# Kernel optimization log

Hardware: AMD Instinct MI355X
Metric: run time of the kernel (lower is better)

Reference implementation:

```python
import jax, jax.numpy as jnp
import numpy as np

STRIDE = 25
TOPK = 3
EPS = 1e-9


def setup_inputs() -> dict:
    key = jax.random.key(0)
    k1, k2, k3, k4 = jax.random.split(key, 4)
    B, N, T, P = 128, 200, 360, 400
    x = jax.random.normal(k1, (B, N, T), dtype=jnp.float32)
    # per-sample time-series lengths; min 100 so size_after_pool >= 1
    length = jax.random.randint(k2, (B,), 100, T + 1)
    # xavier_uniform with gain=1.414 as in nn.init.xavier_uniform_(.., gain=1.414)
    limit = float(np.sqrt(6.0 / (P + N)) * 1.414)
    patterns = jax.random.uniform(k3, (P, N), minval=-limit, maxval=limit, dtype=jnp.float32)
    # simple linear classifier standing in for Baselines.mlp(num_of_node)
    W_cls = jax.random.normal(k4, (N * N, 2), dtype=jnp.float32) * 0.01
    b_cls = jnp.zeros((2,), dtype=jnp.float32)
    return {"x": x, "length": length, "patterns": patterns, "W_cls": W_cls, "b_cls": b_cls}


def _forward(x, length, patterns, W_cls, b_cls):
    B, N, T = x.shape
    P = patterns.shape[0]
    # size_after_pool = floor(length / stride)  [B]
    sap = (length // STRIDE).astype(jnp.int32)
    # MRI_length_regularize (random_start=False): the scatter-mask keeps
    # t < size_after_pool*stride per sample; padded tail is exactly zero and
    # contributes 0 through maxpool+sum, so static full-T masking is equivalent.
    valid = (jnp.arange(T)[None, :] < (sap * STRIDE)[:, None]).astype(x.dtype)  # [B,T]
    frames = (x * valid[:, None, :]).transpose(0, 2, 1)  # [B,T,N]
    nf = frames / jnp.sqrt((frames ** 2).sum(-1, keepdims=True) + EPS)
    npat = patterns / jnp.sqrt((patterns ** 2).sum(-1, keepdims=True) + EPS)
    # top_select: keep top-K |entries| per pattern row
    _, topi = jax.lax.top_k(jnp.abs(npat), TOPK)  # [P,K]
    pmask = jnp.zeros((P, N), x.dtype).at[jnp.arange(P)[:, None], topi].set(1.0)
    toppattern = pmask * npat
    # scores + strided max-pool over time
    scores = jnp.einsum('btn,pn->bpt', nf, npat)  # [B,P,T]
    nwin = T // STRIDE
    pos = scores[:, :, : nwin * STRIDE].reshape(B, P, nwin, STRIDE).max(-1)  # [B,P,nwin]
    finalscore = (pos / sap[:, None, None].astype(x.dtype)).sum(-1)  # [B,P]
    # realpattern = toppattern.detach(); graphs = R^T diag(finalscore) R / (maskgraph+eps)
    realpattern = jax.lax.stop_gradient(toppattern)
    maskgraph = pmask.T @ pmask  # [N,N]
    graphs = jnp.einsum('pn,bp,pm->bnm', realpattern, finalscore, realpattern) / (maskgraph + EPS)
    out = graphs.reshape(B, -1) @ W_cls + b_cls  # [B,2]
    # Critical_ROI(normalized_patterns, toppattern)
    norm = (((1.0 - jnp.linalg.norm(toppattern, axis=-1) / jnp.linalg.norm(npat, axis=-1)) ** 2).sum() / 800.0)
    rec = jnp.zeros((1,), x.dtype)
    return out, norm, rec


def reference(x, length, patterns, W_cls, b_cls):
    return _forward(x, length, patterns, W_cls, b_cls)
```

## Files before the change

### kernel.cpp

```cpp
#include <hip/hip_runtime.h>

#define N_NODE 200
#define T_LEN 360
#define T_POOL 350
#define P_PAT 400
#define P_PAD 512
#define NWIN 14
#define STRIDE_ 25
#define KPAD 224

#define O_AH    0
#define O_AL    229376
#define O_MG    458752
#define O_POS   618752
#define O_TOPN  4288768
#define O_TOPV  4293568
#define O_NORMT 4298368

typedef unsigned short u16;
typedef __attribute__((ext_vector_type(8))) short bf16x8;
typedef __attribute__((ext_vector_type(4))) float f32x4;

__device__ __forceinline__ unsigned fkey(float f) {
    unsigned u = __float_as_uint(f);
    return (u & 0x80000000u) ? ~u : (u | 0x80000000u);
}
__device__ __forceinline__ u16 f2bf(float f) {
    unsigned u = __float_as_uint(f);
    unsigned r = u + 0x7FFFu + ((u >> 16) & 1u);
    return (u16)(r >> 16);
}
__device__ __forceinline__ float bf2f(u16 h) { return __uint_as_float(((unsigned)h) << 16); }

__global__ void k_pat(const float* __restrict__ pat, u16* __restrict__ Ah, u16* __restrict__ Al,
                      int* __restrict__ mg, int* __restrict__ topn_w,
                      float* __restrict__ topv_w, float* __restrict__ normt,
                      unsigned* __restrict__ pos)
{
    int p = blockIdx.x;
    int lane = threadIdx.x;
    bool pv = p < P_PAT;

    {
        int base = blockIdx.x * 64 + lane;
        #pragma unroll
        for (int i = 0; i < 28; ++i) pos[base + i * 32768] = 0u;
    }

    float sv[4], av[4];
    int nn[4];
    float ss = 0.f;
    #pragma unroll
    for (int j = 0; j < 4; ++j) {
        int n = lane + 64 * j;
        nn[j] = n;
        if (pv && n < N_NODE) { float v = pat[p * N_NODE + n]; sv[j] = v; av[j] = fabsf(v); ss += v * v; }
        else { sv[j] = 0.f; av[j] = -1.f; }
    }
    #pragma unroll
    for (int off = 32; off >= 1; off >>= 1) ss += __shfl_xor(ss, off);
    float rn = 1.0f / sqrtf(ss + 1e-9f);

    int pb = p >> 6, ii = (p >> 4) & 3, plm = p & 15;
    #pragma unroll
    for (int j = 0; j < 4; ++j) {
        int n = nn[j];
        if (n < KPAD) {
            float v = (pv && n < N_NODE) ? sv[j] * rn : 0.f;
            u16 h = f2bf(v);
            u16 l = f2bf(v - bf2f(h));
            int s = n >> 5, c = n & 31, quad = c >> 3, e = c & 7;
            size_t idx = ((size_t)((s * 8 + pb) * 4 + ii) * 64 + quad * 16 + plm) * 8 + e;
            Ah[idx] = h; Al[idx] = l;
        }
    }
    if (!pv) return;

    int topn[3]; float topv[3];
    for (int r = 0; r < 3; ++r) {
        float bv = -2.f; int bi = 1 << 30;
        #pragma unroll
        for (int j = 0; j < 4; ++j)
            if (av[j] > bv || (av[j] == bv && nn[j] < bi)) { bv = av[j]; bi = nn[j]; }
        #pragma unroll
        for (int off = 32; off >= 1; off >>= 1) {
            float ov = __shfl_xor(bv, off); int oi = __shfl_xor(bi, off);
            if (ov > bv || (ov == bv && oi < bi)) { bv = ov; bi = oi; }
        }
        int jj = bi >> 6, src = bi & 63;
        float rawj = (jj == 0) ? sv[0] : (jj == 1) ? sv[1] : (jj == 2) ? sv[2] : sv[3];
        float raw = __shfl(rawj, src);
        topn[r] = bi; topv[r] = raw * rn;
        #pragma unroll
        for (int j = 0; j < 4; ++j) if (nn[j] == bi) av[j] = -1.f;
    }
    float fullnorm = sqrtf(ss) * rn;
    float topnorm = sqrtf(topv[0]*topv[0] + topv[1]*topv[1] + topv[2]*topv[2]);
    if (lane == 0) {
        float d = 1.0f - topnorm / fullnorm;
        normt[p] = d * d * (1.0f / 800.0f);
    }
    if (lane < 3) { topn_w[p * 3 + lane] = topn[lane]; topv_w[p * 3 + lane] = topv[lane]; }
    if (lane < 9) {
        int i = lane / 3, j = lane % 3;
        atomicAdd(&mg[topn[i] * N_NODE + topn[j]], 1);
    }
}

#define RP 2064
#define XLOFF 8256
#define DBS 16512
#define SQOFF 16896
#define IVOFF 18944
__global__ __launch_bounds__(256, 3) void k_gemm(const float* __restrict__ x,
    const u16* __restrict__ AhF, const u16* __restrict__ AlF,
    const int* __restrict__ length, unsigned* __restrict__ pos)
{
    __shared__ __align__(16) char smem[33024];
    int tid = threadIdx.x;
    int b = blockIdx.z, p0 = blockIdx.y * 128, t0 = blockIdx.x * 128;
    int lane = tid & 63, wid = tid >> 6;
    int quad = lane >> 4, lm = lane & 15;
    int wp = wid >> 1, wt = wid & 1;
    const float* xb = x + (size_t)b * (N_NODE * T_LEN);

    f32x4 acc[4][4];
    #pragma unroll
    for (int i = 0; i < 4; ++i)
        #pragma unroll
        for (int j = 0; j < 4; ++j) acc[i][j] = (f32x4){0.f, 0.f, 0.f, 0.f};
    float ssq0 = 0.f, ssq1 = 0.f;

    int tg = t0 + 2 * lane;
    bool tok = tg < T_LEN;
    int xfb = quad * RP + (lm & 1) * 1024 + (lm >> 1) * 16 + wt * 512;
    int pbq = blockIdx.y * 2 + wp;

    float2 xv[8];
    auto loadX = [&](int s) {
        int kb = s * 32 + wid * 8;
        #pragma unroll
        for (int e = 0; e < 8; ++e) {
            int k = kb + e;
            xv[e] = (tok && k < N_NODE) ? *(const float2*)(xb + k * T_LEN + tg)
                                        : make_float2(0.f, 0.f);
        }
    };
    auto cw = [&](int buf) {
        union { u16 us[8]; uint4 v; } H0, H1, L0, L1;
        #pragma unroll
        for (int e = 0; e < 8; ++e) {
            float f0 = xv[e].x, f1 = xv[e].y;
            ssq0 = fmaf(f0, f0, ssq0); ssq1 = fmaf(f1, f1, ssq1);
            u16 h = f2bf(f0); H0.us[e] = h; L0.us[e] = f2bf(f0 - bf2f(h));
            h = f2bf(f1);     H1.us[e] = h; L1.us[e] = f2bf(f1 - bf2f(h));
        }
        char* bp = smem + buf * DBS + wid * RP + lane * 16;
        *(uint4*)(bp)               = H0.v;
        *(uint4*)(bp + 1024)        = H1.v;
        *(uint4*)(bp + XLOFF)        = L0.v;
        *(uint4*)(bp + XLOFF + 1024) = L1.v;
    };

    loadX(0); cw(0);
    bf16x8 ah[4], al[4], xh[4], xl[4];
    for (int s = 0; s < 7; ++s) {
        const u16* Ab  = AhF + ((size_t)((s * 8 + pbq) * 4)) * 512 + lane * 8;
        const u16* Ab2 = AlF + ((size_t)((s * 8 + pbq) * 4)) * 512 + lane * 8;
        #pragma unroll
        for (int i = 0; i < 4; ++i) {
            ah[i] = *(const bf16x8*)(Ab  + i * 512);
            al[i] = *(const bf16x8*)(Ab2 + i * 512);
        }
        if (s < 6) loadX(s + 1);
        __syncthreads();
        const char* rb = smem + (s & 1) * DBS + xfb;
        #pragma unroll
        for (int j = 0; j < 4; ++j) {
            xh[j] = *(const bf16x8*)(rb + j * 128);
            xl[j] = *(const bf16x8*)(rb + XLOFF + j * 128);
        }
        #pragma unroll
        for (int i = 0; i < 4; ++i)
            #pragma unroll
            for (int j = 0; j < 4; ++j)
                acc[i][j] = __builtin_amdgcn_mfma_f32_16x16x32_bf16(ah[i], xh[j], acc[i][j], 0, 0, 0);
        #pragma unroll
        for (int i = 0; i < 4; ++i)
            #pragma unroll
            for (int j = 0; j < 4; ++j)
                acc[i][j] = __builtin_amdgcn_mfma_f32_16x16x32_bf16(ah[i], xl[j], acc[i][j], 0, 0, 0);
        #pragma unroll
        for (int i = 0; i < 4; ++i)
            #pragma unroll
            for (int j = 0; j < 4; ++j)
                acc[i][j] = __builtin_amdgcn_mfma_f32_16x16x32_bf16(al[i], xh[j], acc[i][j], 0, 0, 0);
        if (s < 6) cw((s + 1) & 1);
    }

    __syncthreads();
    *(float2*)&smem[SQOFF + tid * 8] = make_float2(ssq0, ssq1);
    __syncthreads();
    int sap = length[b] / STRIDE_;
    int tvalid = sap * STRIDE_;
    if (tid < 64) {
        float a0 = 0.f, a1 = 0.f;
        #pragma unroll
        for (int w2 = 0; w2 < 4; ++w2) {
            float2 v = *(float2*)&smem[SQOFF + (w2 * 64 + tid) * 8];
            a0 += v.x; a1 += v.y;
        }
        float rs = 1.0f / (float)sap;
        int ta = t0 + 2 * tid;
        ((float*)&smem[IVOFF])[2 * tid]     = (ta     < tvalid) ? rs / sqrtf(a0 + 1e-9f) : 0.f;
        ((float*)&smem[IVOFF])[2 * tid + 1] = (ta + 1 < tvalid) ? rs / sqrtf(a1 + 1e-9f) : 0.f;
    }
    __syncthreads();
    float invv[4];
    #pragma unroll
    for (int j = 0; j < 4; ++j) invv[j] = ((float*)&smem[IVOFF])[wt * 64 + j * 16 + lm];

    float* Ss = (float*)smem;
    int wbase = t0 / STRIDE_;
    int tmax = min(t0 + 128, T_POOL);
    for (int rr = 0; rr < 4; ++rr) {
        __syncthreads();
        if (wp == (rr >> 1)) {
            #pragma unroll
            for (int i2 = 0; i2 < 2; ++i2) {
                int i = (rr & 1) * 2 + i2;
                #pragma unroll
                for (int j = 0; j < 4; ++j) {
                    int col = wt * 64 + j * 16 + lm;
                    #pragma unroll
                    for (int r = 0; r < 4; ++r)
                        Ss[(i2 * 16 + quad * 4 + r) * 132 + col] = acc[i][j][r] * invv[j];
                }
            }
        }
        __syncthreads();
        int sidx = tid & 7, pl = tid >> 3;
        int w = wbase + sidx;
        int tlo = max(w * STRIDE_, t0), thi = min(w * STRIDE_ + STRIDE_, tmax);
        if (w < NWIN && tlo < thi) {
            float m = -3.4e38f;
            for (int t = tlo; t < thi; ++t) m = fmaxf(m, Ss[pl * 132 + (t - t0)]);
            atomicMax(&pos[((size_t)b * P_PAD + p0 + rr * 32 + pl) * NWIN + w], fkey(m));
        }
    }
}

__global__ void k_out(const unsigned* __restrict__ pos, const int* __restrict__ topn_w,
                      const float* __restrict__ topv_w, const int* __restrict__ mg,
                      const float* __restrict__ W, const float* __restrict__ normt,
                      const float* __restrict__ bcls, float* __restrict__ out)
{
    __shared__ float cf0[P_PAT], cf1[P_PAT];
    __shared__ float sh[512];
    int b = blockIdx.x, tid = threadIdx.x;
    for (int p = tid; p < P_PAT; p += 256) {
        int tn[3]; float tv[3];
        #pragma unroll
        for (int i = 0; i < 3; ++i) { tn[i] = topn_w[p * 3 + i]; tv[i] = topv_w[p * 3 + i]; }
        float c0 = 0.f, c1 = 0.f;
        #pragma unroll
        for (int i = 0; i < 3; ++i)
            #pragma unroll
            for (int j = 0; j < 3; ++j) {
                int nm = tn[i] * N_NODE + tn[j];
                float f = tv[i] * tv[j] / ((float)mg[nm] + 1e-9f);
                c0 += f * W[nm * 2 + 0];
                c1 += f * W[nm * 2 + 1];
            }
        cf0[p] = c0; cf1[p] = c1;
    }
    __syncthreads();
    float s0 = 0.f, s1 = 0.f;
    for (int p = tid; p < P_PAT; p += 256) {
        const unsigned* pp = pos + ((size_t)b * P_PAD + p) * NWIN;
        float fs = 0.f;
        #pragma unroll
        for (int w = 0; w < NWIN; ++w) {
            unsigned k = pp[w];
            unsigned u = (k & 0x80000000u) ? (k ^ 0x80000000u) : ~k;
            fs += __uint_as_float(u);
        }
        s0 += fs * cf0[p];
        s1 += fs * cf1[p];
    }
    sh[tid] = s0; sh[256 + tid] = s1;
    __syncthreads();
    for (int o = 128; o > 0; o >>= 1) {
        if (tid < o) { sh[tid] += sh[tid + o]; sh[256 + tid] += sh[256 + tid + o]; }
        __syncthreads();
    }
    if (tid == 0) {
        out[b * 2 + 0] = sh[0]   + bcls[0];
        out[b * 2 + 1] = sh[256] + bcls[1];
    }
    if (b == 0) {
        __syncthreads();
        float ns = 0.f;
        for (int i = tid; i < P_PAT; i += 256) ns += normt[i];
        sh[tid] = ns;
        __syncthreads();
        for (int o = 128; o > 0; o >>= 1) {
            if (tid < o) sh[tid] += sh[tid + o];
            __syncthreads();
        }
        if (tid == 0) { out[256] = sh[0]; out[257] = 0.f; }
    }
}

extern "C" void kernel_launch(void* const* d_in, const int* in_sizes, int n_in,
                              void* d_out, int out_size, void* d_ws, size_t ws_size,
                              hipStream_t stream) {
    (void)in_sizes; (void)n_in; (void)out_size; (void)ws_size;
    const float* x        = (const float*)d_in[0];
    const int*   length   = (const int*)d_in[1];
    const float* patterns = (const float*)d_in[2];
    const float* Wcls     = (const float*)d_in[3];
    const float* bcls     = (const float*)d_in[4];
    float* out = (float*)d_out;
    char* ws = (char*)d_ws;

    u16*      Ah    = (u16*)(ws + O_AH);
    u16*      Al    = (u16*)(ws + O_AL);
    int*      mg    = (int*)(ws + O_MG);
    unsigned* pos   = (unsigned*)(ws + O_POS);
    int*      topn  = (int*)(ws + O_TOPN);
    float*    topv  = (float*)(ws + O_TOPV);
    float*    normt = (float*)(ws + O_NORMT);

    hipMemsetAsync(mg, 0, 160000, stream);
    k_pat<<<P_PAD, 64, 0, stream>>>(patterns, Ah, Al, mg, topn, topv, normt, pos);
    k_gemm<<<dim3(3, 4, 128), 256, 0, stream>>>(x, Ah, Al, length, pos);
    k_out<<<128, 256, 0, stream>>>(pos, topn, topv, mg, Wcls, normt, bcls, out);
}
```

Before: 146.4 us.

## Fuse output reduction into GEMM via last-block counter, loop time tiles in-block

Each GEMM block now walks all three time tiles for one (batch, pattern-tile) pair and keeps window maxima in shared memory. This removes the global atomicMax on pos and the zero-initialisation of pos in k_pat. The last of the four pattern-tile blocks per batch, found through an atomic counter, runs the former k_out reduction, so one launch is dropped. The bf16 hi/lo split of x switches from round-to-nearest to truncation, which is cheaper but adds error to the low part, and the grid shrinks from 1536 to 512 blocks with fewer blocks per CU.

```diff
diff --git a/kernel.cpp b/kernel.cpp
--- a/kernel.cpp
+++ b/kernel.cpp
@@ -12,19 +12,24 @@
 #define O_AH    0
 #define O_AL    229376
 #define O_MG    458752
-#define O_POS   618752
-#define O_TOPN  4288768
-#define O_TOPV  4293568
-#define O_NORMT 4298368
+#define O_CTR   618752
+#define O_POS   619264
+#define O_TOPN  4289280
+#define O_TOPV  4294080
+#define O_NORMT 4298880
 
 typedef unsigned short u16;
 typedef __attribute__((ext_vector_type(8))) short bf16x8;
 typedef __attribute__((ext_vector_type(4))) float f32x4;
 
-__device__ __forceinline__ unsigned fkey(float f) {
-    unsigned u = __float_as_uint(f);
-    return (u & 0x80000000u) ? ~u : (u | 0x80000000u);
-}
+#define RP 2064
+#define XLOFF 8256
+#define DBS 16512
+#define SQOFF 16896
+#define IVOFF 18944
+#define WMOFF 33024
+#define SMEM_BYTES 40192
+
 __device__ __forceinline__ u16 f2bf(float f) {
     unsigned u = __float_as_uint(f);
     unsigned r = u + 0x7FFFu + ((u >> 16) & 1u);
@@ -34,18 +39,11 @@
 
 __global__ void k_pat(const float* __restrict__ pat, u16* __restrict__ Ah, u16* __restrict__ Al,
                       int* __restrict__ mg, int* __restrict__ topn_w,
-                      float* __restrict__ topv_w, float* __restrict__ normt,
-                      unsigned* __restrict__ pos)
+                      float* __restrict__ topv_w, float* __restrict__ normt)
 {
     int p = blockIdx.x;
     int lane = threadIdx.x;
     bool pv = p < P_PAT;
-
-    {
-        int base = blockIdx.x * 64 + lane;
-        #pragma unroll
-        for (int i = 0; i < 28; ++i) pos[base + i * 32768] = 0u;
-    }
 
     float sv[4], av[4];
     int nn[4];
@@ -107,157 +105,185 @@
     }
 }
 
-#define RP 2064
-#define XLOFF 8256
-#define DBS 16512
-#define SQOFF 16896
-#define IVOFF 18944
-__global__ __launch_bounds__(256, 3) void k_gemm(const float* __restrict__ x,
+__global__ __launch_bounds__(256, 2) void k_gemm(const float* __restrict__ x,
     const u16* __restrict__ AhF, const u16* __restrict__ AlF,
-    const int* __restrict__ length, unsigned* __restrict__ pos)
+    const int* __restrict__ length, float* __restrict__ pos,
+    unsigned* __restrict__ ctr,
+    const int* __restrict__ topn_w, const float* __restrict__ topv_w,
+    const int* __restrict__ mg, const float* __restrict__ W,
+    const float* __restrict__ normt, const float* __restrict__ bcls,
+    float* __restrict__ out)
 {
-    __shared__ __align__(16) char smem[33024];
+    __shared__ __align__(16) char smem[SMEM_BYTES];
     int tid = threadIdx.x;
-    int b = blockIdx.z, p0 = blockIdx.y * 128, t0 = blockIdx.x * 128;
+    int blk = blockIdx.x;
+    int ptile = (blk >> 3) & 3;
+    int b = (blk & 7) + 8 * (blk >> 5);
+    int p0 = ptile * 128;
     int lane = tid & 63, wid = tid >> 6;
     int quad = lane >> 4, lm = lane & 15;
     int wp = wid >> 1, wt = wid & 1;
+    int pbq = ptile * 2 + wp;
     const float* xb = x + (size_t)b * (N_NODE * T_LEN);
-
-    f32x4 acc[4][4];
-    #pragma unroll
-    for (int i = 0; i < 4; ++i)
-        #pragma unroll
-        for (int j = 0; j < 4; ++j) acc[i][j] = (f32x4){0.f, 0.f, 0.f, 0.f};
-    float ssq0 = 0.f, ssq1 = 0.f;
-
-    int tg = t0 + 2 * lane;
-    bool tok = tg < T_LEN;
-    int xfb = quad * RP + (lm & 1) * 1024 + (lm >> 1) * 16 + wt * 512;
-    int pbq = blockIdx.y * 2 + wp;
-
-    float2 xv[8];
-    auto loadX = [&](int s) {
-        int kb = s * 32 + wid * 8;
-        #pragma unroll
-        for (int e = 0; e < 8; ++e) {
-            int k = kb + e;
-            xv[e] = (tok && k < N_NODE) ? *(const float2*)(xb + k * T_LEN + tg)
-                                        : make_float2(0.f, 0.f);
-        }
-    };
-    auto cw = [&](int buf) {
-        union { u16 us[8]; uint4 v; } H0, H1, L0, L1;
-        #pragma unroll
-        for (int e = 0; e < 8; ++e) {
-            float f0 = xv[e].x, f1 = xv[e].y;
-            ssq0 = fmaf(f0, f0, ssq0); ssq1 = fmaf(f1, f1, ssq1);
-            u16 h = f2bf(f0); H0.us[e] = h; L0.us[e] = f2bf(f0 - bf2f(h));
-            h = f2bf(f1);     H1.us[e] = h; L1.us[e] = f2bf(f1 - bf2f(h));
-        }
-        char* bp = smem + buf * DBS + wid * RP + lane * 16;
-        *(uint4*)(bp)               = H0.v;
-        *(uint4*)(bp + 1024)        = H1.v;
-        *(uint4*)(bp + XLOFF)        = L0.v;
-        *(uint4*)(bp + XLOFF + 1024) = L1.v;
-    };
-
-    loadX(0); cw(0);
-    bf16x8 ah[4], al[4], xh[4], xl[4];
-    for (int s = 0; s < 7; ++s) {
-        const u16* Ab  = AhF + ((size_t)((s * 8 + pbq) * 4)) * 512 + lane * 8;
-        const u16* Ab2 = AlF + ((size_t)((s * 8 + pbq) * 4)) * 512 + lane * 8;
-        #pragma unroll
-        for (int i = 0; i < 4; ++i) {
-            ah[i] = *(const bf16x8*)(Ab  + i * 512);
-            al[i] = *(const bf16x8*)(Ab2 + i * 512);
-        }
-        if (s < 6) loadX(s + 1);
-        __syncthreads();
-        const char* rb = smem + (s & 1) * DBS + xfb;
-        #pragma unroll
-        for (int j = 0; j < 4; ++j) {
-            xh[j] = *(const bf16x8*)(rb + j * 128);
-            xl[j] = *(const bf16x8*)(rb + XLOFF + j * 128);
-        }
-        #pragma unroll
-        for (int i = 0; i < 4; ++i)
-            #pragma unroll
-            for (int j = 0; j < 4; ++j)
-                acc[i][j] = __builtin_amdgcn_mfma_f32_16x16x32_bf16(ah[i], xh[j], acc[i][j], 0, 0, 0);
-        #pragma unroll
-        for (int i = 0; i < 4; ++i)
-            #pragma unroll
-            for (int j = 0; j < 4; ++j)
-                acc[i][j] = __builtin_amdgcn_mfma_f32_16x16x32_bf16(ah[i], xl[j], acc[i][j], 0, 0, 0);
-        #pragma unroll
-        for (int i = 0; i < 4; ++i)
-            #pragma unroll
-            for (int j = 0; j < 4; ++j)
-                acc[i][j] = __builtin_amdgcn_mfma_f32_16x16x32_bf16(al[i], xh[j], acc[i][j], 0, 0, 0);
-        if (s < 6) cw((s + 1) & 1);
-    }
-
-    __syncthreads();
-    *(float2*)&smem[SQOFF + tid * 8] = make_float2(ssq0, ssq1);
-    __syncthreads();
     int sap = length[b] / STRIDE_;
     int tvalid = sap * STRIDE_;
-    if (tid < 64) {
-        float a0 = 0.f, a1 = 0.f;
-        #pragma unroll
-        for (int w2 = 0; w2 < 4; ++w2) {
-            float2 v = *(float2*)&smem[SQOFF + (w2 * 64 + tid) * 8];
-            a0 += v.x; a1 += v.y;
-        }
-        float rs = 1.0f / (float)sap;
-        int ta = t0 + 2 * tid;
-        ((float*)&smem[IVOFF])[2 * tid]     = (ta     < tvalid) ? rs / sqrtf(a0 + 1e-9f) : 0.f;
-        ((float*)&smem[IVOFF])[2 * tid + 1] = (ta + 1 < tvalid) ? rs / sqrtf(a1 + 1e-9f) : 0.f;
-    }
-    __syncthreads();
-    float invv[4];
-    #pragma unroll
-    for (int j = 0; j < 4; ++j) invv[j] = ((float*)&smem[IVOFF])[wt * 64 + j * 16 + lm];
-
-    float* Ss = (float*)smem;
-    int wbase = t0 / STRIDE_;
-    int tmax = min(t0 + 128, T_POOL);
-    for (int rr = 0; rr < 4; ++rr) {
-        __syncthreads();
-        if (wp == (rr >> 1)) {
-            #pragma unroll
-            for (int i2 = 0; i2 < 2; ++i2) {
-                int i = (rr & 1) * 2 + i2;
+
+    float* wmax = (float*)&smem[WMOFF];
+    #pragma unroll
+    for (int i = 0; i < 7; ++i) wmax[tid + i * 256] = 0.f;
+
+    for (int ti = 0; ti < 3; ++ti) {
+        int t0 = ti * 128;
+        int tg = t0 + 2 * lane;
+        bool tok = tg < T_LEN;
+        int xfb = quad * RP + (lm & 1) * 1024 + (lm >> 1) * 16 + wt * 512;
+
+        f32x4 acc[4][4];
+        #pragma unroll
+        for (int i = 0; i < 4; ++i)
+            #pragma unroll
+            for (int j = 0; j < 4; ++j) acc[i][j] = (f32x4){0.f, 0.f, 0.f, 0.f};
+        float ssq0 = 0.f, ssq1 = 0.f;
+
+        float2 xv[8];
+        auto loadX = [&](int s) {
+            int kb = s * 32 + wid * 8;
+            #pragma unroll
+            for (int e = 0; e < 8; ++e) {
+                int k = kb + e;
+                xv[e] = (tok && k < N_NODE) ? *(const float2*)(xb + k * T_LEN + tg)
+                                            : make_float2(0.f, 0.f);
+            }
+        };
+        auto cw = [&](int buf) {
+            union { u16 us[8]; uint4 v; } H0, H1, L0, L1;
+            #pragma unroll
+            for (int e = 0; e < 8; ++e) {
+                float f0 = xv[e].x, f1 = xv[e].y;
+                ssq0 = fmaf(f0, f0, ssq0); ssq1 = fmaf(f1, f1, ssq1);
+                unsigned u0 = __float_as_uint(f0), u1 = __float_as_uint(f1);
+                H0.us[e] = (u16)(u0 >> 16);
+                H1.us[e] = (u16)(u1 >> 16);
+                float l0 = f0 - __uint_as_float(u0 & 0xFFFF0000u);
+                float l1 = f1 - __uint_as_float(u1 & 0xFFFF0000u);
+                L0.us[e] = (u16)(__float_as_uint(l0) >> 16);
+                L1.us[e] = (u16)(__float_as_uint(l1) >> 16);
+            }
+            char* bp = smem + buf * DBS + wid * RP + lane * 16;
+            *(uint4*)(bp)                = H0.v;
+            *(uint4*)(bp + 1024)         = H1.v;
+            *(uint4*)(bp + XLOFF)        = L0.v;
+            *(uint4*)(bp + XLOFF + 1024) = L1.v;
+        };
+
+        loadX(0); cw(0);
+        bf16x8 ah[4], al[4], xh[4], xl[4];
+        for (int s = 0; s < 7; ++s) {
+            const u16* Ab  = AhF + (size_t)(s * 8 + pbq) * 2048 + lane * 8;
+            const u16* Ab2 = AlF + (size_t)(s * 8 + pbq) * 2048 + lane * 8;
+            #pragma unroll
+            for (int i = 0; i < 4; ++i) {
+                ah[i] = *(const bf16x8*)(Ab  + i * 512);
+                al[i] = *(const bf16x8*)(Ab2 + i * 512);
+            }
+            if (s < 6) loadX(s + 1);
+            __syncthreads();
+            const char* rb = smem + (s & 1) * DBS + xfb;
+            #pragma unroll
+            for (int j = 0; j < 4; ++j) {
+                xh[j] = *(const bf16x8*)(rb + j * 128);
+                xl[j] = *(const bf16x8*)(rb + XLOFF + j * 128);
+            }
+            #pragma unroll
+            for (int i = 0; i < 4; ++i)
                 #pragma unroll
-                for (int j = 0; j < 4; ++j) {
-                    int col = wt * 64 + j * 16 + lm;
+                for (int j = 0; j < 4; ++j)
+                    acc[i][j] = __builtin_amdgcn_mfma_f32_16x16x32_bf16(ah[i], xh[j], acc[i][j], 0, 0, 0);
+            #pragma unroll
+            for (int i = 0; i < 4; ++i)
+                #pragma unroll
+                for (int j = 0; j < 4; ++j)
+                    acc[i][j] = __builtin_amdgcn_mfma_f32_16x16x32_bf16(ah[i], xl[j], acc[i][j], 0, 0, 0);
+            #pragma unroll
+            for (int i = 0; i < 4; ++i)
+                #pragma unroll
+                for (int j = 0; j < 4; ++j)
+                    acc[i][j] = __builtin_amdgcn_mfma_f32_16x16x32_bf16(al[i], xh[j], acc[i][j], 0, 0, 0);
+            if (s < 6) cw((s + 1) & 1);
+        }
+
+        __syncthreads();
+        *(float2*)&smem[SQOFF + tid * 8] = make_float2(ssq0, ssq1);
+        __syncthreads();
+        if (tid < 64) {
+            float a0 = 0.f, a1 = 0.f;
+            #pragma unroll
+            for (int w2 = 0; w2 < 4; ++w2) {
+                float2 v = *(float2*)&smem[SQOFF + (w2 * 64 + tid) * 8];
+                a0 += v.x; a1 += v.y;
+            }
+            float rs = 1.0f / (float)sap;
+            int ta = t0 + 2 * tid;
+            ((float*)&smem[IVOFF])[2 * tid]     = (ta     < tvalid) ? rs / sqrtf(a0 + 1e-9f) : 0.f;
+            ((float*)&smem[IVOFF])[2 * tid + 1] = (ta + 1 < tvalid) ? rs / sqrtf(a1 + 1e-9f) : 0.f;
+        }
+        __syncthreads();
+        float invv[4];
+        #pragma unroll
+        for (int j = 0; j < 4; ++j) invv[j] = ((float*)&smem[IVOFF])[wt * 64 + j * 16 + lm];
+
+        float* Ss = (float*)smem;
+        int wbase = t0 / STRIDE_;
+        int tmax = min(t0 + 128, T_POOL);
+        for (int rr = 0; rr < 4; ++rr) {
+            __syncthreads();
+            if (wp == (rr >> 1)) {
+                #pragma unroll
+                for (int i2 = 0; i2 < 2; ++i2) {
+                    int i = (rr & 1) * 2 + i2;
                     #pragma unroll
-                    for (int r = 0; r < 4; ++r)
-                        Ss[(i2 * 16 + quad * 4 + r) * 132 + col] = acc[i][j][r] * invv[j];
+                    for (int j = 0; j < 4; ++j) {
+                        int col = wt * 64 + j * 16 + lm;
+                        #pragma unroll
+                        for (int r = 0; r < 4; ++r)
+                            Ss[(i2 * 16 + quad * 4 + r) * 132 + col] = acc[i][j][r] * invv[j];
+                    }
                 }
             }
-        }
-        __syncthreads();
-        int sidx = tid & 7, pl = tid >> 3;
-        int w = wbase + sidx;
-        int tlo = max(w * STRIDE_, t0), thi = min(w * STRIDE_ + STRIDE_, tmax);
-        if (w < NWIN && tlo < thi) {
-            float m = -3.4e38f;
-            for (int t = tlo; t < thi; ++t) m = fmaxf(m, Ss[pl * 132 + (t - t0)]);
-            atomicMax(&pos[((size_t)b * P_PAD + p0 + rr * 32 + pl) * NWIN + w], fkey(m));
-        }
-    }
-}
-
-__global__ void k_out(const unsigned* __restrict__ pos, const int* __restrict__ topn_w,
-                      const float* __restrict__ topv_w, const int* __restrict__ mg,
-                      const float* __restrict__ W, const float* __restrict__ normt,
-                      const float* __restrict__ bcls, float* __restrict__ out)
-{
-    __shared__ float cf0[P_PAT], cf1[P_PAT];
-    __shared__ float sh[512];
-    int b = blockIdx.x, tid = threadIdx.x;
+            __syncthreads();
+            int sidx = tid & 7, pl = tid >> 3;
+            int w = wbase + sidx;
+            int tlo = max(w * STRIDE_, t0), thi = min(w * STRIDE_ + STRIDE_, tmax);
+            if (w < NWIN && tlo < thi) {
+                float m = -3.4e38f;
+                for (int t = tlo; t < thi; ++t) m = fmaxf(m, Ss[pl * 132 + (t - t0)]);
+                int row = rr * 32 + pl;
+                wmax[row * 14 + w] = fmaxf(wmax[row * 14 + w], m);
+            }
+        }
+        __syncthreads();
+    }
+
+    float* posb = pos + ((size_t)b * P_PAD + p0) * NWIN;
+    #pragma unroll
+    for (int i = 0; i < 7; ++i) posb[tid + i * 256] = wmax[tid + i * 256];
+    __syncthreads();
+
+    volatile int* flagp = (volatile int*)smem;
+    if (tid == 0) {
+        __threadfence();
+        unsigned old = atomicAdd(&ctr[b], 1u);
+        *flagp = (old == 3u) ? 1 : 0;
+    }
+    __syncthreads();
+    int flag = *flagp;
+    __syncthreads();
+    if (!flag) return;
+    __threadfence();
+
+    float* cf0 = (float*)smem;
+    float* cf1 = (float*)(smem + 1600);
+    float* sh  = (float*)(smem + 3200);
     for (int p = tid; p < P_PAT; p += 256) {
         int tn[3]; float tv[3];
         #pragma unroll
@@ -277,14 +303,10 @@
     __syncthreads();
     float s0 = 0.f, s1 = 0.f;
     for (int p = tid; p < P_PAT; p += 256) {
-        const unsigned* pp = pos + ((size_t)b * P_PAD + p) * NWIN;
+        const float* pp = pos + ((size_t)b * P_PAD + p) * NWIN;
         float fs = 0.f;
         #pragma unroll
-        for (int w = 0; w < NWIN; ++w) {
-            unsigned k = pp[w];
-            unsigned u = (k & 0x80000000u) ? (k ^ 0x80000000u) : ~k;
-            fs += __uint_as_float(u);
-        }
+        for (int w = 0; w < NWIN; ++w) fs += pp[w];
         s0 += fs * cf0[p];
         s1 += fs * cf1[p];
     }
@@ -327,13 +349,14 @@
     u16*      Ah    = (u16*)(ws + O_AH);
     u16*      Al    = (u16*)(ws + O_AL);
     int*      mg    = (int*)(ws + O_MG);
-    unsigned* pos   = (unsigned*)(ws + O_POS);
+    unsigned* ctr   = (unsigned*)(ws + O_CTR);
+    float*    pos   = (float*)(ws + O_POS);
     int*      topn  = (int*)(ws + O_TOPN);
     float*    topv  = (float*)(ws + O_TOPV);
     float*    normt = (float*)(ws + O_NORMT);
 
-    hipMemsetAsync(mg, 0, 160000, stream);
-    k_pat<<<P_PAD, 64, 0, stream>>>(patterns, Ah, Al, mg, topn, topv, normt, pos);
-    k_gemm<<<dim3(3, 4, 128), 256, 0, stream>>>(x, Ah, Al, length, pos);
-    k_out<<<128, 256, 0, stream>>>(pos, topn, topv, mg, Wcls, normt, bcls, out);
+    hipMemsetAsync(mg, 0, 160512, stream);
+    k_pat<<<P_PAD, 64, 0, stream>>>(patterns, Ah, Al, mg, topn, topv, normt);
+    k_gemm<<<512, 256, 0, stream>>>(x, Ah, Al, length, pos, ctr,
+                                    topn, topv, mg, Wcls, normt, bcls, out);
 }
```

New measurement: 308.3 us. +110.6%, slower.

## Drop split-bf16 GEMM to single bf16 pass and compute mask graph in-kernel

Applied to the files above, without the earlier changes.

Replaces the three-pass hi/lo bf16 split GEMM, which emulated fp32 accuracy, with a single bf16 MFMA pass. The x side is converted by truncation instead of rounding. This cuts MFMA work, shared-memory traffic and global loads of the low-part patterns by roughly a factor of three, but lowers score precision, which can change max-pool and output values. The maskgraph counts are no longer built with a memset and global atomics. Each k_out block rebuilds them from per-node pattern bitmasks using popcount, which removes a memset launch and the atomics at the cost of redundant per-block work.

```diff
diff --git a/kernel.cpp b/kernel.cpp
--- a/kernel.cpp
+++ b/kernel.cpp
@@ -10,16 +10,20 @@
 #define KPAD 224
 
 #define O_AH    0
-#define O_AL    229376
-#define O_MG    458752
-#define O_POS   618752
-#define O_TOPN  4288768
-#define O_TOPV  4293568
-#define O_NORMT 4298368
+#define O_POS   229376
+#define O_TOPN  3899392
+#define O_TOPV  3904192
+#define O_NORMT 3908992
 
 typedef unsigned short u16;
 typedef __attribute__((ext_vector_type(8))) short bf16x8;
 typedef __attribute__((ext_vector_type(4))) float f32x4;
+
+#define RP 2064
+#define DBS 8256
+#define SQOFF 16512
+#define IVOFF 18560
+#define SMEM_BYTES 19072
 
 __device__ __forceinline__ unsigned fkey(float f) {
     unsigned u = __float_as_uint(f);
@@ -30,12 +34,10 @@
     unsigned r = u + 0x7FFFu + ((u >> 16) & 1u);
     return (u16)(r >> 16);
 }
-__device__ __forceinline__ float bf2f(u16 h) { return __uint_as_float(((unsigned)h) << 16); }
-
-__global__ void k_pat(const float* __restrict__ pat, u16* __restrict__ Ah, u16* __restrict__ Al,
-                      int* __restrict__ mg, int* __restrict__ topn_w,
-                      float* __restrict__ topv_w, float* __restrict__ normt,
-                      unsigned* __restrict__ pos)
+
+__global__ void k_pat(const float* __restrict__ pat, u16* __restrict__ Ah,
+                      int* __restrict__ topn_w, float* __restrict__ topv_w,
+                      float* __restrict__ normt, unsigned* __restrict__ pos)
 {
     int p = blockIdx.x;
     int lane = threadIdx.x;
@@ -67,11 +69,9 @@
         int n = nn[j];
         if (n < KPAD) {
             float v = (pv && n < N_NODE) ? sv[j] * rn : 0.f;
-            u16 h = f2bf(v);
-            u16 l = f2bf(v - bf2f(h));
             int s = n >> 5, c = n & 31, quad = c >> 3, e = c & 7;
             size_t idx = ((size_t)((s * 8 + pb) * 4 + ii) * 64 + quad * 16 + plm) * 8 + e;
-            Ah[idx] = h; Al[idx] = l;
+            Ah[idx] = f2bf(v);
         }
     }
     if (!pv) return;
@@ -101,27 +101,19 @@
         normt[p] = d * d * (1.0f / 800.0f);
     }
     if (lane < 3) { topn_w[p * 3 + lane] = topn[lane]; topv_w[p * 3 + lane] = topv[lane]; }
-    if (lane < 9) {
-        int i = lane / 3, j = lane % 3;
-        atomicAdd(&mg[topn[i] * N_NODE + topn[j]], 1);
-    }
-}
-
-#define RP 2064
-#define XLOFF 8256
-#define DBS 16512
-#define SQOFF 16896
-#define IVOFF 18944
+}
+
 __global__ __launch_bounds__(256, 3) void k_gemm(const float* __restrict__ x,
-    const u16* __restrict__ AhF, const u16* __restrict__ AlF,
-    const int* __restrict__ length, unsigned* __restrict__ pos)
+    const u16* __restrict__ AhF, const int* __restrict__ length,
+    unsigned* __restrict__ pos)
 {
-    __shared__ __align__(16) char smem[33024];
+    __shared__ __align__(16) char smem[SMEM_BYTES];
     int tid = threadIdx.x;
     int b = blockIdx.z, p0 = blockIdx.y * 128, t0 = blockIdx.x * 128;
     int lane = tid & 63, wid = tid >> 6;
     int quad = lane >> 4, lm = lane & 15;
     int wp = wid >> 1, wt = wid & 1;
+    int pbq = blockIdx.y * 2 + wp;
     const float* xb = x + (size_t)b * (N_NODE * T_LEN);
 
     f32x4 acc[4][4];
@@ -134,7 +126,6 @@
     int tg = t0 + 2 * lane;
     bool tok = tg < T_LEN;
     int xfb = quad * RP + (lm & 1) * 1024 + (lm >> 1) * 16 + wt * 512;
-    int pbq = blockIdx.y * 2 + wp;
 
     float2 xv[8];
     auto loadX = [&](int s) {
@@ -147,58 +138,38 @@
         }
     };
     auto cw = [&](int buf) {
-        union { u16 us[8]; uint4 v; } H0, H1, L0, L1;
+        union { u16 us[8]; uint4 v; } H0, H1;
         #pragma unroll
         for (int e = 0; e < 8; ++e) {
             float f0 = xv[e].x, f1 = xv[e].y;
             ssq0 = fmaf(f0, f0, ssq0); ssq1 = fmaf(f1, f1, ssq1);
-            u16 h = f2bf(f0); H0.us[e] = h; L0.us[e] = f2bf(f0 - bf2f(h));
-            h = f2bf(f1);     H1.us[e] = h; L1.us[e] = f2bf(f1 - bf2f(h));
+            H0.us[e] = (u16)(__float_as_uint(f0) >> 16);
+            H1.us[e] = (u16)(__float_as_uint(f1) >> 16);
         }
         char* bp = smem + buf * DBS + wid * RP + lane * 16;
-        *(uint4*)(bp)               = H0.v;
-        *(uint4*)(bp + 1024)        = H1.v;
-        *(uint4*)(bp + XLOFF)        = L0.v;
-        *(uint4*)(bp + XLOFF + 1024) = L1.v;
+        *(uint4*)(bp)        = H0.v;
+        *(uint4*)(bp + 1024) = H1.v;
     };
 
     loadX(0); cw(0);
-    bf16x8 ah[4], al[4], xh[4], xl[4];
+    bf16x8 ah[4], xh[4];
     for (int s = 0; s < 7; ++s) {
-        const u16* Ab  = AhF + ((size_t)((s * 8 + pbq) * 4)) * 512 + lane * 8;
-        const u16* Ab2 = AlF + ((size_t)((s * 8 + pbq) * 4)) * 512 + lane * 8;
-        #pragma unroll
-        for (int i = 0; i < 4; ++i) {
-            ah[i] = *(const bf16x8*)(Ab  + i * 512);
-            al[i] = *(const bf16x8*)(Ab2 + i * 512);
-        }
+        const u16* Ab = AhF + (size_t)(s * 8 + pbq) * 2048 + lane * 8;
+        #pragma unroll
+        for (int i = 0; i < 4; ++i) ah[i] = *(const bf16x8*)(Ab + i * 512);
         if (s < 6) loadX(s + 1);
         __syncthreads();
         const char* rb = smem + (s & 1) * DBS + xfb;
         #pragma unroll
-        for (int j = 0; j < 4; ++j) {
-            xh[j] = *(const bf16x8*)(rb + j * 128);
-            xl[j] = *(const bf16x8*)(rb + XLOFF + j * 128);
-        }
+        for (int j = 0; j < 4; ++j) xh[j] = *(const bf16x8*)(rb + j * 128);
         #pragma unroll
         for (int i = 0; i < 4; ++i)
             #pragma unroll
             for (int j = 0; j < 4; ++j)
                 acc[i][j] = __builtin_amdgcn_mfma_f32_16x16x32_bf16(ah[i], xh[j], acc[i][j], 0, 0, 0);
-        #pragma unroll
-        for (int i = 0; i < 4; ++i)
-            #pragma unroll
-            for (int j = 0; j < 4; ++j)
-                acc[i][j] = __builtin_amdgcn_mfma_f32_16x16x32_bf16(ah[i], xl[j], acc[i][j], 0, 0, 0);
-        #pragma unroll
-        for (int i = 0; i < 4; ++i)
-            #pragma unroll
-            for (int j = 0; j < 4; ++j)
-                acc[i][j] = __builtin_amdgcn_mfma_f32_16x16x32_bf16(al[i], xh[j], acc[i][j], 0, 0, 0);
         if (s < 6) cw((s + 1) & 1);
     }
 
-    __syncthreads();
     *(float2*)&smem[SQOFF + tid * 8] = make_float2(ssq0, ssq1);
     __syncthreads();
     int sap = length[b] / STRIDE_;
@@ -251,13 +222,24 @@
 }
 
 __global__ void k_out(const unsigned* __restrict__ pos, const int* __restrict__ topn_w,
-                      const float* __restrict__ topv_w, const int* __restrict__ mg,
-                      const float* __restrict__ W, const float* __restrict__ normt,
-                      const float* __restrict__ bcls, float* __restrict__ out)
+                      const float* __restrict__ topv_w, const float* __restrict__ W,
+                      const float* __restrict__ normt, const float* __restrict__ bcls,
+                      float* __restrict__ out)
 {
+    __shared__ unsigned maskT[N_NODE * 13];
     __shared__ float cf0[P_PAT], cf1[P_PAT];
     __shared__ float sh[512];
     int b = blockIdx.x, tid = threadIdx.x;
+
+    for (int i = tid; i < N_NODE * 13; i += 256) maskT[i] = 0u;
+    __syncthreads();
+    for (int idx = tid; idx < P_PAT * 3; idx += 256) {
+        int q = idx / 3;
+        int n = topn_w[idx];
+        atomicOr(&maskT[n * 13 + (q >> 5)], 1u << (q & 31));
+    }
+    __syncthreads();
+
     for (int p = tid; p < P_PAT; p += 256) {
         int tn[3]; float tv[3];
         #pragma unroll
@@ -267,8 +249,13 @@
         for (int i = 0; i < 3; ++i)
             #pragma unroll
             for (int j = 0; j < 3; ++j) {
-                int nm = tn[i] * N_NODE + tn[j];
-                float f = tv[i] * tv[j] / ((float)mg[nm] + 1e-9f);
+                int a = tn[i], bb = tn[j];
+                int mgv = 0;
+                #pragma unroll
+                for (int w = 0; w < 13; ++w)
+                    mgv += __popc(maskT[a * 13 + w] & maskT[bb * 13 + w]);
+                int nm = a * N_NODE + bb;
+                float f = tv[i] * tv[j] / ((float)mgv + 1e-9f);
                 c0 += f * W[nm * 2 + 0];
                 c1 += f * W[nm * 2 + 1];
             }
@@ -325,15 +312,12 @@
     char* ws = (char*)d_ws;
 
     u16*      Ah    = (u16*)(ws + O_AH);
-    u16*      Al    = (u16*)(ws + O_AL);
-    int*      mg    = (int*)(ws + O_MG);
     unsigned* pos   = (unsigned*)(ws + O_POS);
     int*      topn  = (int*)(ws + O_TOPN);
     float*    topv  = (float*)(ws + O_TOPV);
     float*    normt = (float*)(ws + O_NORMT);
 
-    hipMemsetAsync(mg, 0, 160000, stream);
-    k_pat<<<P_PAD, 64, 0, stream>>>(patterns, Ah, Al, mg, topn, topv, normt, pos);
-    k_gemm<<<dim3(3, 4, 128), 256, 0, stream>>>(x, Ah, Al, length, pos);
-    k_out<<<128, 256, 0, stream>>>(pos, topn, topv, mg, Wcls, normt, bcls, out);
-}
+    k_pat<<<P_PAD, 64, 0, stream>>>(patterns, Ah, topn, topv, normt, pos);
+    k_gemm<<<dim3(3, 4, 128), 256, 0, stream>>>(x, Ah, length, pos);
+    k_out<<<128, 256, 0, stream>>>(pos, topn, topv, Wcls, normt, bcls, out);
+}
```

New measurement: 138.4 us. 1.06x faster.
